# Kernel tuning notes

Measured on AMD Instinct MI355X. Metric: run time of the kernel, lower is better.

## Reference

```python
import jax, jax.numpy as jnp
import numpy as np

SIGMA = 0.02
B, CC, H, W = 4, 21, 96, 96
C_LOW, C_HIGH = 3, 512
N = H * W


def _grid_edges(h, w):
    idx = np.arange(h * w).reshape(h, w)
    eh = np.stack([idx[:, :-1].ravel(), idx[:, 1:].ravel()], 1)
    ev = np.stack([idx[:-1, :].ravel(), idx[1:, :].ravel()], 1)
    return np.concatenate([eh, ev], 0)  # [E,2] 4-connected grid edges


def _mst_bfs(feat, h, w):
    # feat: [C,h,w] numpy. Kruskal MST with norm2 edge weights, then BFS from node 0.
    n = h * w
    edges = _grid_edges(h, w)
    f = feat.reshape(feat.shape[0], -1)
    wts = ((f[:, edges[:, 0]] - f[:, edges[:, 1]]) ** 2).sum(0)
    order = np.argsort(wts, kind='stable')
    uf = np.arange(n)

    def find(x):
        r = x
        while uf[r] != r:
            r = uf[r]
        while uf[x] != r:
            uf[x], x = r, uf[x]
        return r

    adj = [[] for _ in range(n)]
    cnt = 0
    for ei in order:
        a, b = int(edges[ei, 0]), int(edges[ei, 1])
        ra, rb = find(a), find(b)
        if ra != rb:
            uf[ra] = rb
            adj[a].append(b)
            adj[b].append(a)
            cnt += 1
            if cnt == n - 1:
                break
    parent = np.zeros(n, np.int64)
    seen = np.zeros(n, bool)
    seen[0] = True
    levels, frontier = [[0]], [0]
    while frontier:
        nxt = []
        for u in frontier:
            for v in adj[u]:
                if not seen[v]:
                    seen[v] = True
                    parent[v] = u
                    nxt.append(v)
        if nxt:
            levels.append(nxt)
        frontier = nxt
    return parent, levels


def _tree_arrays(embed):
    # Host-side MST + BFS level schedule (integer tree topology, non-differentiable).
    e = np.asarray(jax.device_get(embed)).astype(np.float64)
    bn = e.shape[0]
    parents, levels = [], []
    for b in range(bn):
        p, lv = _mst_bfs(e[b], H, W)
        parents.append(p)
        levels.append(lv)
    D = max(len(lv) for lv in levels)
    L = max(max(len(l) for l in lv) for lv in levels)
    nodes = np.full((bn, D, L), N, np.int32)  # index N = dummy sink node
    for b, lv in enumerate(levels):
        for d, l in enumerate(lv):
            nodes[b, d, :len(l)] = l
    par = np.stack(parents)
    par = np.concatenate([par, np.full((bn, 1), N)], 1).astype(np.int32)
    msk = np.ones((bn, N + 1), np.float32)
    msk[:, 0] = 0.0  # root has no parent edge
    msk[:, N] = 0.0  # dummy node
    return jnp.asarray(nodes), jnp.asarray(par), jnp.asarray(msk)


def _tree_filter(feat, embed, nodes, parent, wmask, sigma):
    # feat [B,C,N], embed [B,Ce,N]. O(N) two-pass (leaf->root, root->leaf) tree DP:
    # out_i = sum_j (prod_{e in path(i,j)} w_e) f_j / same-with-f=1
    bn, c, nn = feat.shape
    ez = jnp.pad(embed, ((0, 0), (0, 0), (0, 1)))  # add dummy column
    ep = jax.vmap(lambda e, p: e[:, p])(ez, parent)  # parent embedding [B,Ce,N+1]
    w = wmask * jnp.exp(-((ez - ep) ** 2).sum(1) / sigma)  # edge weight per node [B,N+1]
    fa = jnp.concatenate([feat, jnp.ones((bn, 1, nn), feat.dtype)], 1)  # append norm channel
    fa = jnp.pad(fa, ((0, 0), (0, 0), (0, 1)))  # [B,C+1,N+1]

    def one(a0, wv, par, lvls):
        def up(a, lvl):  # children before parents: subtree aggregation
            return a.at[:, par[lvl]].add(wv[lvl] * a[:, lvl]), None
        a, _ = jax.lax.scan(up, a0, lvls[::-1])

        def down(s, lvl):  # parents before children: whole-tree aggregation
            wl = wv[lvl]
            sv = a[:, lvl] + wl * (s[:, par[lvl]] - wl * a[:, lvl])
            return s.at[:, lvl].set(sv), None
        s, _ = jax.lax.scan(down, a, lvls)
        return s

    s = jax.vmap(one)(fa, w, parent, nodes)
    return s[:, :c, :nn] / s[:, c:, :nn]


def _nearest(x, h, w):
    hr, wr = x.shape[-2:]
    ri = jnp.arange(h) * hr // h
    ci = jnp.arange(w) * wr // w
    return x[..., ri[:, None], ci[None, :]]


def setup_inputs():
    key = jax.random.key(0)
    k1, k2, k3, k4 = jax.random.split(key, 4)
    preds = jax.random.normal(k1, (B, CC, H, W), jnp.float32)
    low_feats = jax.random.uniform(k2, (B, C_LOW, H, W), dtype=jnp.float32)
    high_feats = 0.03 * jax.random.normal(k3, (B, C_HIGH, H, W), jnp.float32)
    roi = (jax.random.uniform(k4, (B, 1, 2 * H, 2 * W)) > 0.5).astype(jnp.float32)
    return {'preds': preds, 'low_feats': low_feats, 'high_feats': high_feats,
            'unlabeled_ROIs': roi}


def reference(preds, low_feats, high_feats, unlabeled_ROIs):
    nodes_l, par_l, msk_l = _tree_arrays(low_feats)
    nodes_h, par_h, msk_h = _tree_arrays(high_feats)
    roi = _nearest(unlabeled_ROIs, H, W)
    n = roi.sum()
    prob = jax.nn.sigmoid(preds)
    lf = low_feats.reshape(B, C_LOW, N)
    hf = high_feats.reshape(B, C_HIGH, N)
    AS = _tree_filter(prob.reshape(B, CC, N), lf, nodes_l, par_l, msk_l, SIGMA)
    AS = _tree_filter(AS, hf, nodes_h, par_h, msk_h, 1.0)
    loss = (roi * jnp.abs(prob - AS.reshape(B, CC, H, W))).sum()
    return jnp.where(n > 0, loss / n, jnp.zeros_like(loss))
```

## Files before the change

### kernel.cpp

```cpp
#include <hip/hip_runtime.h>
#include <math.h>
#include <stdint.h>
#include <stddef.h>


namespace {
constexpr int Bn  = 4, Cc = 21, Hh = 96, Ww = 96;
constexpr int Nn  = Hh * Ww;
constexpr int EhE = Hh * (Ww - 1);
constexpr int Ne  = EhE + (Hh - 1) * Ww;
constexpr int Clow = 3, Chigh = 512;
constexpr int NCh = Cc + 1;
constexpr int MAXD = 2048;
constexpr int TL  = 2 * (Nn - 1);
constexpr int ESL = 18432;
constexpr int SEG = 19;
constexpr int NR  = (TL + SEG - 1) / SEG;
constexpr int MAXC = 4608;
constexpr int NB_INIT = (Bn * Cc * Nn + 255) / 256;
constexpr int NB_EDGE = (Bn * Ne + 255) / 256;

constexpr size_t OFF_ACC  = 0;
constexpr size_t OFF_PROB = 256;
constexpr size_t OFF_S1   = OFF_PROB + (size_t)Bn * Cc * Nn * 4;
constexpr size_t OFF_S2   = OFF_S1   + (size_t)Bn * NCh * Nn * 4;
constexpr size_t OFF_EW   = OFF_S2   + (size_t)Bn * NCh * Nn * 4;
constexpr size_t OFF_ORD  = OFF_EW   + (size_t)8 * Ne * 8;
constexpr size_t OFF_PPOS = OFF_ORD  + (size_t)8 * Nn * 4;
constexpr size_t OFF_WGT  = OFF_PPOS + (size_t)8 * Nn * 2;
constexpr size_t OFF_LEV  = OFF_WGT  + (size_t)8 * Nn * 4;
constexpr size_t OFF_D    = OFF_LEV  + (size_t)8 * MAXD * 4;
constexpr size_t OFF_DIR  = OFF_D    + 256;
constexpr size_t OFF_CBW  = OFF_DIR  + (size_t)8 * Nn * 4;
constexpr size_t OFF_CBE  = OFF_CBW  + (size_t)8 * Nn * 8;
constexpr size_t OFF_OPP  = OFF_CBE  + (size_t)8 * Nn * 4;
constexpr size_t OFF_SGN  = OFF_OPP  + (size_t)8 * ESL * 2;
constexpr size_t OFF_PNF  = OFF_SGN  + (size_t)8 * ESL;
constexpr size_t OFF_RNK  = OFF_PNF  + (size_t)8 * Nn * 4;
constexpr size_t OFF_PAIR = OFF_RNK  + (size_t)8 * ESL * 2;
constexpr size_t OFF_EL1  = OFF_ORD;
constexpr size_t OFF_EL2  = OFF_WGT;
}

__device__ __forceinline__ void edge_nodes(int e, int& a, int& b) {
    if (e < EhE) { int h = e / (Ww - 1), w = e - h * (Ww - 1); a = h * Ww + w; b = a + 1; }
    else { int e2 = e - EhE; int h = e2 / Ww, w = e2 - h * Ww; a = h * Ww + w; b = a + Ww; }
}
__device__ __forceinline__ int dir_delta(int d) {
    return (d == 0) ? 1 : (d == 1) ? -1 : (d == 2) ? Ww : -Ww;
}
__device__ __forceinline__ int edge_of(int u, int d) {
    int h = u / Ww, w = u - h * Ww;
    if (d == 0) return h * (Ww - 1) + w;
    if (d == 1) return h * (Ww - 1) + w - 1;
    if (d == 2) return EhE + u;
    return EhE + u - Ww;
}

__device__ __forceinline__ unsigned long long mkkey(double w, int e) {
    unsigned long long q = (unsigned long long)(w * 70368744177664.0);
    if (q >= (1ull << 49)) q = (1ull << 49) - 1;
    return (q << 15) | (unsigned)e;
}

__device__ __forceinline__ void compact_push(bool keep, int val, int* cnt,
                                             unsigned short* out, int lane) {
    unsigned long long m = __ballot(keep ? 1 : 0);
    if (m == 0ull) return;
    int leader = __ffsll((unsigned long long)m) - 1;
    int base = 0;
    if (lane == leader) base = atomicAdd(cnt, __popcll(m));
    base = __shfl(base, leader, 64);
    if (keep) {
        unsigned long long lower = m & ((1ull << lane) - 1ull);
        out[base + __popcll(lower)] = (unsigned short)val;
    }
}

__device__ __forceinline__ int scan1024s(int val, int tid, int* wsum) {
    __syncthreads();
    int lane = tid & 63, wv = tid >> 6;
    int x = val;
    #pragma unroll
    for (int off = 1; off < 64; off <<= 1) {
        int y = __shfl_up(x, off, 64);
        if (lane >= off) x += y;
    }
    if (lane == 63) wsum[wv] = x;
    __syncthreads();
    if (wv == 0) {
        int s2 = (lane < 16) ? wsum[lane] : 0;
        #pragma unroll
        for (int off = 1; off < 16; off <<= 1) {
            int y = __shfl_up(s2, off, 64);
            if (lane >= off) s2 += y;
        }
        if (lane < 16) wsum[lane] = s2;
    }
    __syncthreads();
    int base = (wv > 0) ? wsum[wv - 1] : 0;
    return x + base;
}

__device__ __forceinline__ void edgew_body(const float* __restrict__ feat, int C,
                                           double* __restrict__ ew, int idx) {
    if (idx >= Bn * Ne) return;
    int b = idx / Ne, e = idx - b * Ne;
    int a, c2; edge_nodes(e, a, c2);
    const float* fa = feat + (size_t)b * C * Nn + a;
    const float* fb = feat + (size_t)b * C * Nn + c2;
    double s = 0.0;
    int c = 0;
    for (; c + 16 <= C; c += 16) {
        float va[16], vb[16];
        #pragma unroll
        for (int k = 0; k < 16; k++) {
            va[k] = fa[(size_t)(c + k) * Nn];
            vb[k] = fb[(size_t)(c + k) * Nn];
        }
        #pragma unroll
        for (int k = 0; k < 16; k++) {
            double d = (double)va[k] - (double)vb[k];
            s += d * d;
        }
    }
    for (; c < C; c++) {
        double d = (double)fa[(size_t)c * Nn] - (double)fb[(size_t)c * Nn];
        s += d * d;
    }
    ew[idx] = s;
}

__global__ void k_prep(const float* __restrict__ preds,
                       const float* __restrict__ lowf,
                       const float* __restrict__ highf,
                       float* __restrict__ prob, double* __restrict__ acc,
                       double* __restrict__ ewl, double* __restrict__ ewh) {
    int bid = blockIdx.x;
    if (bid < NB_INIT) {
        int idx = bid * 256 + threadIdx.x;
        if (idx == 0) { acc[0] = 0.0; acc[1] = 0.0; }
        if (idx >= Bn * Cc * Nn) return;
        prob[idx] = 1.0f / (1.0f + expf(-preds[idx]));
    } else if (bid < NB_INIT + NB_EDGE) {
        int idx = (bid - NB_INIT) * 256 + threadIdx.x;
        edgew_body(lowf, Clow, ewl, idx);
    } else {
        int idx = (bid - NB_INIT - NB_EDGE) * 256 + threadIdx.x;
        edgew_body(highf, Chigh, ewh, idx);
    }
}

__global__ void __launch_bounds__(1024)
k_mst(char* __restrict__ ws) {
    const int tb = blockIdx.x, tid = threadIdx.x;
    const int lane = tid & 63;
    const double* ew = (const double*)(ws + OFF_EW) + (size_t)tb * Ne;
    int* dirG = (int*)(ws + OFF_DIR) + (size_t)tb * Nn;
    unsigned short* elA = (unsigned short*)(ws + OFF_EL1) + (size_t)tb * Ne;
    unsigned short* elB = (unsigned short*)(ws + OFF_EL2) + (size_t)tb * Ne;

    __shared__ unsigned short comp[Nn];
    __shared__ unsigned long long cbK[MAXC];
    __shared__ int wsumM[16];
    __shared__ int chgArr[48];
    __shared__ int sLen, sNC;

    unsigned short* nxtN     = (unsigned short*)cbK;
    unsigned short* newSlotN = (unsigned short*)cbK + Nn;
    unsigned short* nxt      = (unsigned short*)cbK;
    unsigned short* newSlot  = (unsigned short*)cbK + MAXC;

    for (int i = tid; i < Nn; i += 1024) dirG[i] = 0;
    if (tid < 48) chgArr[tid] = 0;
    __syncthreads();

    for (int i = tid; i < Nn; i += 1024) {
        int h = i / Ww, w = i - h * Ww;
        unsigned long long bk = ~0ull;
        if (w < Ww - 1) { int e = h * (Ww - 1) + w;     unsigned long long k = mkkey(ew[e], e); if (k < bk) bk = k; }
        if (w > 0)      { int e = h * (Ww - 1) + w - 1; unsigned long long k = mkkey(ew[e], e); if (k < bk) bk = k; }
        if (h < Hh - 1) { int e = EhE + i;              unsigned long long k = mkkey(ew[e], e); if (k < bk) bk = k; }
        if (h > 0)      { int e = EhE + i - Ww;         unsigned long long k = mkkey(ew[e], e); if (k < bk) bk = k; }
        int e = (int)(bk & 0x7FFF);
        int a, c; edge_nodes(e, a, c);
        nxtN[i] = (unsigned short)((a == i) ? c : a);
        int da = (c == a + 1) ? 0 : 2;
        atomicOr(&dirG[a], 1 << da);
        atomicOr(&dirG[c], 1 << (da ^ 1));
    }
    __syncthreads();
    for (int i = tid; i < Nn; i += 1024) {
        int o = nxtN[i];
        if (o != i && nxtN[o] == i && i < o) nxtN[i] = (unsigned short)i;
    }
    __syncthreads();
    {
        int it = 0;
        while (it < 40) {
            bool any = false;
            for (int r = tid; r < Nn; r += 1024) {
                int nr = nxtN[r], nnr = nxtN[nr];
                if (nr != nnr) { nxtN[r] = (unsigned short)nnr; any = true; }
            }
            if (any) chgArr[it] = 1;
            __syncthreads();
            if (!chgArr[it]) break;
            it++;
        }
    }
    {
        int base = tid * 9, cnt = 0, loc[9];
        #pragma unroll
        for (int k = 0; k < 9; k++) {
            int i = base + k;
            loc[k] = cnt;
            if (nxtN[i] == i) cnt++;
        }
        int incl = scan1024s(cnt, tid, wsumM);
        int eb = incl - cnt;
        #pragma unroll
        for (int k = 0; k < 9; k++) {
            int i = base + k;
            if (nxtN[i] == i) newSlotN[i] = (unsigned short)(eb + loc[k]);
        }
        if (tid == 1023) sNC = incl;
    }
    __syncthreads();
    for (int i = tid; i < Nn; i += 1024) comp[i] = newSlotN[nxtN[i]];
    __syncthreads();
    int nComp = sNC;

    unsigned short* src = elA;
    unsigned short* dst = elB;
    int srcLen = -1;
    for (int round = 2; round < 22 && nComp > 1; round++) {
        if (tid == 0) sLen = 0;
        if (tid < 48) chgArr[tid] = 0;
        __syncthreads();
        if (srcLen < 0) {
            for (int e = tid; e < Ne; e += 1024) {
                int a, c; edge_nodes(e, a, c);
                compact_push(comp[a] != comp[c], e, &sLen, dst, lane);
            }
        } else {
            for (int k = tid; k < srcLen; k += 1024) {
                int e = src[k];
                int a, c; edge_nodes(e, a, c);
                compact_push(comp[a] != comp[c], e, &sLen, dst, lane);
            }
        }
        for (int s = tid; s < nComp; s += 1024) cbK[s] = ~0ull;
        __syncthreads();
        int len = sLen;
        if (len == 0) break;
        for (int k = tid; k < len; k += 1024) {
            int e = dst[k];
            int a, c; edge_nodes(e, a, c);
            unsigned long long key = mkkey(ew[e], e);
            atomicMin(&cbK[comp[a]], key);
            atomicMin(&cbK[comp[c]], key);
        }
        __syncthreads();
        unsigned long long kr[5];
        int nOwn = 0;
        for (int s = tid; s < nComp; s += 1024) kr[nOwn++] = cbK[s];
        __syncthreads();
        {
            int o = 0;
            for (int s = tid; s < nComp; s += 1024, o++) {
                unsigned long long key = kr[o];
                if (key != ~0ull) {
                    int e = (int)(key & 0x7FFF);
                    int a, c; edge_nodes(e, a, c);
                    int sa = comp[a], sc = comp[c];
                    nxt[s] = (unsigned short)((sa == s) ? sc : sa);
                    int da = (c == a + 1) ? 0 : 2;
                    atomicOr(&dirG[a], 1 << da);
                    atomicOr(&dirG[c], 1 << (da ^ 1));
                } else nxt[s] = (unsigned short)s;
            }
        }
        __syncthreads();
        for (int s = tid; s < nComp; s += 1024) {
            int o = nxt[s];
            if (o != s && nxt[o] == s && s < o) nxt[s] = (unsigned short)s;
        }
        __syncthreads();
        {
            int it = 0;
            while (it < 40) {
                bool any = false;
                for (int s = tid; s < nComp; s += 1024) {
                    int ns = nxt[s], nns = nxt[ns];
                    if (ns != nns) { nxt[s] = (unsigned short)nns; any = true; }
                }
                if (any) chgArr[it] = 1;
                __syncthreads();
                if (!chgArr[it]) break;
                it++;
            }
        }
        {
            int K = (nComp + 1023) >> 10;
            int base = tid * K, cnt = 0, loc[5];
            for (int k = 0; k < K; k++) {
                int s = base + k;
                loc[k] = cnt;
                if (s < nComp && nxt[s] == s) cnt++;
            }
            int incl = scan1024s(cnt, tid, wsumM);
            int eb = incl - cnt;
            for (int k = 0; k < K; k++) {
                int s = base + k;
                if (s < nComp && nxt[s] == s) newSlot[s] = (unsigned short)(eb + loc[k]);
            }
            if (tid == 1023) sNC = incl;
        }
        __syncthreads();
        for (int i = tid; i < Nn; i += 1024) comp[i] = newSlot[nxt[comp[i]]];
        __syncthreads();
        nComp = sNC;
        unsigned short* t = src; src = dst; dst = t;
        srcLen = len;
    }
}

__global__ void __launch_bounds__(1024)
k_topo(char* __restrict__ ws) {
    const int tb = blockIdx.x, tid = threadIdx.x;
    const int lane = tid & 63, wv = tid >> 6;
    const int tree = tb >> 2;
    const double* ew  = (const double*)(ws + OFF_EW) + (size_t)tb * Ne;
    const int*  dirG  = (const int*)(ws + OFF_DIR) + (size_t)tb * Nn;
    unsigned int*   elemSegG = (unsigned int*)(ws + OFF_CBW + (size_t)tb * 73728);
    unsigned short* ORG      = (unsigned short*)(ws + OFF_CBW + (size_t)tb * 73728);
    unsigned short* OWNR     = ORG + ESL;
    unsigned short* ownG     = (unsigned short*)(ws + OFF_CBE + (size_t)tb * (size_t)ESL * 2);
    unsigned short* oppG     = (unsigned short*)(ws + OFF_OPP + (size_t)tb * (size_t)ESL * 2);
    unsigned short* IRG      = (unsigned short*)(ws + OFF_SGN + (size_t)tb * ESL);
    unsigned short* rank0G   = (unsigned short*)(ws + OFF_RNK + (size_t)tb * (size_t)ESL * 2);
    int*            ordG  = (int*)(ws + OFF_ORD)  + (size_t)tb * Nn;
    uint2*          pairG = (uint2*)(ws + OFF_PAIR) + (size_t)tb * Nn;
    int*            levG  = (int*)(ws + OFF_LEV)  + (size_t)tb * MAXD;
    int*            dG    = (int*)(ws + OFF_D);
    const float inv_sigma = tree ? 1.0f : 50.0f;

    __shared__ char A[36864];
    __shared__ char B[18432];
    __shared__ char C[9216];
    __shared__ int  wsum[16];
    __shared__ int  sR, sPack, sCenter;

    unsigned short* degOff = (unsigned short*)B;
    unsigned char*  nbS    = (unsigned char*)C;
    for (int i = tid; i < Nn; i += 1024) nbS[i] = (unsigned char)dirG[i];
    __syncthreads();
    {
        int base9 = tid * 9;
        int loc[9]; int s = 0;
        #pragma unroll
        for (int k = 0; k < 9; k++) { loc[k] = s; s += __popc(nbS[base9 + k]); }
        int incl = scan1024s(s, tid, wsum);
        int eb = incl - s;
        #pragma unroll
        for (int k = 0; k < 9; k++) degOff[base9 + k] = (unsigned short)(eb + loc[k]);
    }
    __syncthreads();

    unsigned short* nxtS = (unsigned short*)A;
    for (int u = tid; u < Nn; u += 1024) {
        int m = nbS[u]; int base = degOff[u]; int k = 0;
        #pragma unroll
        for (int d = 0; d < 4; d++) {
            if (m & (1 << d)) {
                int v = u + dir_delta(d);
                int mv = nbS[v]; int rd = d ^ 1;
                int pv = __popc(mv & ((1 << rd) - 1));
                int dv = __popc(mv);
                int nx = pv + 1; if (nx == dv) nx = 0;
                int j = base + k;
                nxtS[j] = (unsigned short)(degOff[v] + nx);
                ownG[j] = (unsigned short)((u << 2) | d);
                oppG[j] = (unsigned short)(degOff[v] + pv);
                k++;
            }
        }
    }
    __syncthreads();

    int myNr = 0, myLen = 0;
    if (tid < NR) {
        int x = tid * SEG, off = 0;
        for (int g = 0; g < 4096; g++) {
            elemSegG[x] = ((unsigned)tid << 11) | (unsigned)off;
            int y = nxtS[x];
            if (y % SEG == 0) { myNr = y / SEG; myLen = off + 1; break; }
            x = y; off++;
        }
    }
    __syncthreads();

    unsigned short* cn  = (unsigned short*)C;
    unsigned short* cd  = (unsigned short*)(C + 2048);
    unsigned short* nn2 = (unsigned short*)(C + 4096);
    unsigned short* nd2 = (unsigned short*)(C + 6144);
    if (tid == 0)      { cn[0] = 0; cd[0] = 0; }
    else if (tid < NR) { cn[tid] = (unsigned short)myNr; cd[tid] = (unsigned short)myLen; }
    else               { cn[tid] = (unsigned short)tid; cd[tid] = 0; }
    __syncthreads();
    for (int r = 0; r < 10; r++) {
        int c = cn[tid];
        int dv = cd[tid] + cd[c];
        int n2 = cn[c];
        nn2[tid] = (unsigned short)n2; nd2[tid] = (unsigned short)dv;
        __syncthreads();
        unsigned short* t;
        t = cn; cn = nn2; nn2 = t;
        t = cd; cd = nd2; nd2 = t;
    }
    unsigned short* rb = nn2;
    rb[tid] = (tid == 0) ? 0 : (unsigned short)(TL - cd[tid]);
    __syncthreads();

    for (int hh = 0; hh < 2; hh++) {
        unsigned int pk4[9];
        #pragma unroll
        for (int t = 0; t < 9; t++) {
            int e = tid + (hh * 9 + t) * 1024;
            pk4[t] = elemSegG[e < TL ? e : 0];
        }
        unsigned short rbv[9];
        #pragma unroll
        for (int t = 0; t < 9; t++) rbv[t] = rb[pk4[t] >> 11];
        #pragma unroll
        for (int t = 0; t < 9; t++) {
            int e = tid + (hh * 9 + t) * 1024;
            if (e < TL) rank0G[e] = (unsigned short)(rbv[t] + (pk4[t] & 2047));
        }
    }
    __syncthreads();

    for (int hh = 0; hh < 2; hh++) {
        unsigned short rnk[9], opp[9], own2[9];
        #pragma unroll
        for (int t = 0; t < 9; t++) {
            int j = tid + (hh * 9 + t) * 1024;
            int ja = j < TL ? j : 0;
            rnk[t] = rank0G[ja]; opp[t] = oppG[ja]; own2[t] = ownG[ja];
        }
        unsigned short r2[9];
        #pragma unroll
        for (int t = 0; t < 9; t++) r2[t] = rank0G[opp[t]];
        #pragma unroll
        for (int t = 0; t < 9; t++) {
            int j = tid + (hh * 9 + t) * 1024;
            if (j < TL) { int r = rnk[t]; ORG[r] = r2[t]; OWNR[r] = own2[t]; }
        }
    }
    {
        unsigned short dof[9];
        #pragma unroll
        for (int t = 0; t < 9; t++) dof[t] = degOff[tid + t * 1024];
        unsigned short ov[9];
        #pragma unroll
        for (int t = 0; t < 9; t++) ov[t] = oppG[dof[t]];
        unsigned short rv[9];
        #pragma unroll
        for (int t = 0; t < 9; t++) rv[t] = rank0G[ov[t]];
        #pragma unroll
        for (int t = 0; t < 9; t++) IRG[tid + t * 1024] = rv[t];
    }
    __syncthreads();

    short* scanS = (short*)A;
    unsigned char* parC = (unsigned char*)C;
    unsigned short* depthB = (unsigned short*)B;
    int curRoot = 0, rootC = 0;
    for (int ph = 0; ph < 3; ph++) {
        if (tid == 0) {
            sR = ORG[IRG[curRoot]];
            sPack = 0;
        }
        __syncthreads();
        const int R = sR;
        const bool doPar = (ph >= 1);
        int base = tid * 18;
        int n = TL - base; if (n > 18) n = 18; if (n < 0) n = 0;
        unsigned short orvA[18], ownA[18];
        #pragma unroll
        for (int k = 0; k < 18; k++) {
            int q = base + k;
            int r = q + R; if (r >= TL) r -= TL; if (q >= TL) r = 0;
            orvA[k] = ORG[r];
        }
        if (doPar) {
            #pragma unroll
            for (int k = 0; k < 18; k++) {
                int q = base + k;
                int r = q + R; if (r >= TL) r -= TL; if (q >= TL) r = 0;
                ownA[k] = OWNR[r];
            }
        }
        short loc[18]; int s = 0;
        #pragma unroll
        for (int k = 0; k < 18; k++) {
            if (k < n) {
                int q = base + k;
                int rro = (int)orvA[k] - R; if (rro < 0) rro += TL;
                bool desc = q < rro;
                if (doPar && desc) {
                    int own = ownA[k];
                    int head = (own >> 2) + dir_delta(own & 3);
                    parC[head] = (unsigned char)((own & 3) ^ 1);
                }
                s += desc ? 1 : -1;
                loc[k] = (short)s;
            }
        }
        int incl = scan1024s(s, tid, wsum);
        int eb = incl - s;
        #pragma unroll
        for (int k = 0; k < 18; k++)
            if (k < n) scanS[base + k] = (short)(loc[k] + eb);
        __syncthreads();
        int pk = 0;
        {
            unsigned short qA[9];
            #pragma unroll
            for (int j = 0; j < 9; j++) qA[j] = IRG[tid + j * 1024];
            int depA[9];
            #pragma unroll
            for (int j = 0; j < 9; j++) {
                int q = (int)qA[j] - R; if (q < 0) q += TL;
                depA[j] = (int)scanS[q];
            }
            #pragma unroll
            for (int j = 0; j < 9; j++) {
                int x = tid + j * 1024;
                int dep = (x == curRoot) ? 0 : depA[j];
                int p2 = (dep << 14) | x;
                if (p2 > pk) pk = p2;
                if (ph == 2) depthB[x] = (unsigned short)dep;
            }
        }
        #pragma unroll
        for (int off = 32; off > 0; off >>= 1) {
            int o = __shfl_down(pk, off, 64);
            if (o > pk) pk = o;
        }
        if (lane == 0) atomicMax(&sPack, pk);
        __syncthreads();
        if (ph == 0) curRoot = sPack & 16383;
        else if (ph == 1) {
            int diam = sPack >> 14, v = sPack & 16383;
            int steps = diam - (diam >> 1);
            unsigned short* J  = (unsigned short*)A;
            unsigned short* J2 = (unsigned short*)(A + 18432);
            for (int x = tid; x < Nn; x += 1024)
                J[x] = (unsigned short)((x == curRoot) ? x : (x + dir_delta(parC[x])));
            if (tid == 0) sCenter = v;
            __syncthreads();
            for (int k = 0; (steps >> k) != 0; k++) {
                if (tid == 0 && ((steps >> k) & 1)) sCenter = J[sCenter];
                if ((steps >> (k + 1)) != 0) {
                    __syncthreads();
                    for (int x = tid; x < Nn; x += 1024) J2[x] = J[J[x]];
                    __syncthreads();
                    unsigned short* t = J; J = J2; J2 = t;
                }
            }
            __syncthreads();
            curRoot = sCenter;
            rootC = curRoot;
        }
        __syncthreads();
    }
    const int D = (sPack >> 14) + 1;

    unsigned short* posOf = (unsigned short*)A;
    int* hist   = (int*)(A + 18432);
    int* levOff = (int*)(A + 26624);
    for (int k = tid; k < 2048; k += 1024) hist[k] = 0;
    __syncthreads();
    for (int v = tid; v < Nn; v += 1024) atomicAdd(&hist[depthB[v]], 1);
    __syncthreads();
    {
        int h0 = hist[2 * tid], h1 = hist[2 * tid + 1];
        int partial = h0 + h1;
        int incl = scan1024s(partial, tid, wsum);
        int eb = incl - partial;
        levOff[2 * tid] = eb;
        levOff[2 * tid + 1] = eb + h0;
    }
    __syncthreads();
    for (int d = tid; d <= D && d < 2048; d += 1024) levG[d] = levOff[d];
    for (int k = tid; k < 2048; k += 1024) hist[k] = 0;
    __syncthreads();
    for (int v = tid; v < Nn; v += 1024) {
        int dep = depthB[v];
        int pos = levOff[dep] + atomicAdd(&hist[dep], 1);
        posOf[v] = (unsigned short)pos;
        ordG[pos] = v;
    }
    __syncthreads();

    {
        unsigned char rdA[9]; unsigned short posA[9];
        #pragma unroll
        for (int t = 0; t < 9; t++) {
            int v = tid + t * 1024;
            rdA[t] = parC[v]; posA[t] = posOf[v];
        }
        double ewv[9]; unsigned short ppv[9];
        #pragma unroll
        for (int t = 0; t < 9; t++) {
            int v = tid + t * 1024;
            int rd = rdA[t] & 3;
            bool ir = (v == rootC);
            int p  = ir ? v : v + dir_delta(rd);
            int ei = ir ? 0 : edge_of(v, rd);
            ppv[t] = posOf[p];
            ewv[t] = ew[ei];
        }
        #pragma unroll
        for (int t = 0; t < 9; t++) {
            int v = tid + t * 1024;
            int pos = posA[t];
            if (v == rootC) {
                pairG[pos] = make_uint2(0u, 0u);
            } else {
                float w = expf(-(float)ewv[t] * inv_sigma);
                pairG[pos] = make_uint2(__float_as_uint(w), (unsigned)ppv[t]);
            }
        }
    }
    if (tid == 0) dG[tb] = D;
}

__global__ void __launch_bounds__(64)
k_dp(char* __restrict__ ws, int tree, int inMode) {
    const int bc = blockIdx.x;
    const int b = bc / NCh, c = bc % NCh;
    const int tb = tree * Bn + b;
    const int lane = threadIdx.x;
    const int*   ordG  = (const int*)(ws + OFF_ORD)  + (size_t)tb * Nn;
    const uint2* pairG = (const uint2*)(ws + OFF_PAIR) + (size_t)tb * Nn;
    const int*   levG  = (const int*)(ws + OFF_LEV)  + (size_t)tb * MAXD;
    const int D = ((const int*)(ws + OFF_D))[tb];
    const float* src = (inMode == 0)
        ? (const float*)(ws + OFF_PROB) + ((size_t)b * Cc + c) * Nn
        : (const float*)(ws + OFF_S1)   + ((size_t)b * NCh + c) * Nn;
    const float* srcN = (const float*)(ws + OFF_S1) + ((size_t)b * NCh + Cc) * Nn;
    float* dst = (float*)(ws + (tree ? OFF_S2 : OFF_S1)) + ((size_t)b * NCh + c) * Nn;

    __shared__ alignas(16) float Al[Nn];
    __shared__ alignas(16) uint2 pairS[Nn];
    __shared__ unsigned short levS[MAXD];

    {
        const uint4* pg4 = (const uint4*)pairG;
        uint4* ps4 = (uint4*)pairS;
        for (int k = lane; k < Nn / 2; k += 64) ps4[k] = pg4[k];
    }
    for (int d = lane; d <= D && d < MAXD; d += 64) levS[d] = (unsigned short)levG[d];
    if (c == Cc)            { for (int i = lane; i < Nn; i += 64) Al[i] = 1.0f; }
    else if (inMode == 0)   { for (int i = lane; i < Nn; i += 64) Al[i] = src[ordG[i]]; }
    else                    { for (int i = lane; i < Nn; i += 64) { int nd = ordG[i]; Al[i] = src[nd] / srcN[nd]; } }
    __builtin_amdgcn_wave_barrier();
    asm volatile("" ::: "memory");

    if (D > 1) {
        for (int d = D - 1; d >= 1; d--) {
            int sd = levS[d], sd1 = levS[d + 1];
            for (int i = sd + lane; i < sd1; i += 64) {
                uint2 pk = pairS[i];
                atomicAdd(&Al[pk.y], __uint_as_float(pk.x) * Al[i]);
            }
        }
    }
    if (D > 1) {
        for (int d = 1; d < D; d++) {
            int sd = levS[d], sd1 = levS[d + 1];
            for (int i = sd + lane; i < sd1; i += 64) {
                uint2 pk = pairS[i];
                float w = __uint_as_float(pk.x);
                float a = Al[i];
                Al[i] = a + w * (Al[pk.y] - w * a);
            }
        }
    }
    __builtin_amdgcn_wave_barrier();
    asm volatile("" ::: "memory");
    for (int i = lane; i < Nn; i += 64) dst[ordG[i]] = Al[i];
}

__global__ void k_loss(char* __restrict__ ws, const float* __restrict__ roi) {
    const int tid = threadIdx.x;
    int idx = blockIdx.x * 256 + tid;
    const float* prob = (const float*)(ws + OFF_PROB);
    const float* S2   = (const float*)(ws + OFF_S2);
    double* acc = (double*)(ws + OFF_ACC);
    double ls = 0.0, cnt = 0.0;
    if (idx < Bn * Cc * Nn) {
        int b = idx / (Cc * Nn);
        int rem = idx - b * (Cc * Nn);
        int c = rem / Nn, n = rem - c * Nn;
        int h = n / Ww, w2 = n - h * Ww;
        float r = roi[(size_t)b * (2 * Hh) * (2 * Ww) + (size_t)(2 * h) * (2 * Ww) + 2 * w2];
        float as = S2[((size_t)b * NCh + c) * Nn + n] / S2[((size_t)b * NCh + Cc) * Nn + n];
        float pp = prob[((size_t)b * Cc + c) * Nn + n];
        ls = (double)(r * fabsf(pp - as));
        if (c == 0) cnt = (double)r;
    }
    __shared__ double sl[256], sc2[256];
    sl[tid] = ls; sc2[tid] = cnt;
    __syncthreads();
    for (int s = 128; s > 0; s >>= 1) {
        if (tid < s) { sl[tid] += sl[tid + s]; sc2[tid] += sc2[tid + s]; }
        __syncthreads();
    }
    if (tid == 0) { atomicAdd(acc, sl[0]); atomicAdd(acc + 1, sc2[0]); }
}

__global__ void k_final(const double* __restrict__ acc, float* __restrict__ out) {
    if (blockIdx.x == 0 && threadIdx.x == 0)
        out[0] = (acc[1] > 0.0) ? (float)(acc[0] / acc[1]) : 0.0f;
}

extern "C" void kernel_launch(void* const* d_in, const int* in_sizes, int n_in,
                              void* d_out, int out_size, void* d_ws, size_t ws_size,
                              hipStream_t stream) {
    const float* preds = (const float*)d_in[0];
    const float* lowf  = (const float*)d_in[1];
    const float* highf = (const float*)d_in[2];
    const float* roi   = (const float*)d_in[3];
    char* ws = (char*)d_ws;
    float* out = (float*)d_out;
    double* ewl = (double*)(ws + OFF_EW);
    double* ewh = (double*)(ws + OFF_EW) + (size_t)Bn * Ne;

    k_prep<<<NB_INIT + 2 * NB_EDGE, 256, 0, stream>>>(
        preds, lowf, highf, (float*)(ws + OFF_PROB), (double*)(ws + OFF_ACC),
        ewl, ewh);
    k_mst<<<8, 1024, 0, stream>>>(ws);
    k_topo<<<8, 1024, 0, stream>>>(ws);
    k_dp<<<Bn * NCh, 64, 0, stream>>>(ws, 0, 0);
    k_dp<<<Bn * NCh, 64, 0, stream>>>(ws, 1, 1);
    k_loss<<<(Bn * Cc * Nn + 255) / 256, 256, 0, stream>>>(ws, roi);
    k_final<<<1, 64, 0, stream>>>((const double*)(ws + OFF_ACC), out);
}
```

Baseline: 659.1 us.

## Process two tree levels per top-down pass using grandparent pointers

The topology kernel now also stores each node's grandparent position, packed into the pair word, plus the parent's edge weight in a new array. The top-down DP pass handles two levels per step: a node in the second level recomputes its parent's updated value from the grandparent, so half as many level iterations are needed. Chunks are processed in reverse order so that nodes read their parent's value before it is overwritten. This adds another shared array of about 36KB plus extra loads per node, which may lower occupancy, and it depends on OFF_WGT being defined elsewhere.

```diff
diff --git a/kernel.cpp b/kernel.cpp
--- a/kernel.cpp
+++ b/kernel.cpp
@@ -342,6 +342,7 @@
     unsigned short* rank0G   = (unsigned short*)(ws + OFF_RNK + (size_t)tb * (size_t)ESL * 2);
     int*            ordG  = (int*)(ws + OFF_ORD)  + (size_t)tb * Nn;
     uint2*          pairG = (uint2*)(ws + OFF_PAIR) + (size_t)tb * Nn;
+    float*          wpG   = (float*)(ws + OFF_WGT) + (size_t)tb * Nn;
     int*            levG  = (int*)(ws + OFF_LEV)  + (size_t)tb * MAXD;
     int*            dG    = (int*)(ws + OFF_D);
     const float inv_sigma = tree ? 1.0f : 50.0f;
@@ -612,26 +613,46 @@
             int v = tid + t * 1024;
             rdA[t] = parC[v]; posA[t] = posOf[v];
         }
-        double ewv[9]; unsigned short ppv[9];
+        int p1A[9];
         #pragma unroll
         for (int t = 0; t < 9; t++) {
             int v = tid + t * 1024;
-            int rd = rdA[t] & 3;
-            bool ir = (v == rootC);
-            int p  = ir ? v : v + dir_delta(rd);
-            int ei = ir ? 0 : edge_of(v, rd);
-            ppv[t] = posOf[p];
+            p1A[t] = (v == rootC) ? v : v + dir_delta(rdA[t] & 3);
+        }
+        unsigned char rd1A[9];
+        #pragma unroll
+        for (int t = 0; t < 9; t++) rd1A[t] = parC[p1A[t]];
+        int p2A[9];
+        #pragma unroll
+        for (int t = 0; t < 9; t++)
+            p2A[t] = (p1A[t] == rootC) ? p1A[t] : p1A[t] + dir_delta(rd1A[t] & 3);
+        unsigned short pp1[9], pp2[9];
+        #pragma unroll
+        for (int t = 0; t < 9; t++) {
+            pp1[t] = posOf[p1A[t]];
+            pp2[t] = posOf[p2A[t]];
+        }
+        double ewv[9], ewp[9];
+        #pragma unroll
+        for (int t = 0; t < 9; t++) {
+            int v = tid + t * 1024;
+            int ei  = (v == rootC) ? 0 : edge_of(v, rdA[t] & 3);
+            int eip = (p1A[t] == rootC) ? 0 : edge_of(p1A[t], rd1A[t] & 3);
             ewv[t] = ew[ei];
+            ewp[t] = ew[eip];
         }
         #pragma unroll
         for (int t = 0; t < 9; t++) {
             int v = tid + t * 1024;
             int pos = posA[t];
+            wpG[pos] = (p1A[t] == rootC) ? 0.0f
+                     : expf(-(float)ewp[t] * inv_sigma);
             if (v == rootC) {
                 pairG[pos] = make_uint2(0u, 0u);
             } else {
                 float w = expf(-(float)ewv[t] * inv_sigma);
-                pairG[pos] = make_uint2(__float_as_uint(w), (unsigned)ppv[t]);
+                pairG[pos] = make_uint2(__float_as_uint(w),
+                                        (unsigned)pp1[t] | ((unsigned)pp2[t] << 14));
             }
         }
     }
@@ -646,6 +667,7 @@
     const int lane = threadIdx.x;
     const int*   ordG  = (const int*)(ws + OFF_ORD)  + (size_t)tb * Nn;
     const uint2* pairG = (const uint2*)(ws + OFF_PAIR) + (size_t)tb * Nn;
+    const float* wpGp  = (const float*)(ws + OFF_WGT) + (size_t)tb * Nn;
     const int*   levG  = (const int*)(ws + OFF_LEV)  + (size_t)tb * MAXD;
     const int D = ((const int*)(ws + OFF_D))[tb];
     const float* src = (inMode == 0)
@@ -656,12 +678,16 @@
 
     __shared__ alignas(16) float Al[Nn];
     __shared__ alignas(16) uint2 pairS[Nn];
+    __shared__ alignas(16) float wpS[Nn];
     __shared__ unsigned short levS[MAXD];
 
     {
         const uint4* pg4 = (const uint4*)pairG;
         uint4* ps4 = (uint4*)pairS;
         for (int k = lane; k < Nn / 2; k += 64) ps4[k] = pg4[k];
+        const uint4* wg4 = (const uint4*)wpGp;
+        uint4* ws4 = (uint4*)wpS;
+        for (int k = lane; k < Nn / 4; k += 64) ws4[k] = wg4[k];
     }
     for (int d = lane; d <= D && d < MAXD; d += 64) levS[d] = (unsigned short)levG[d];
     if (c == Cc)            { for (int i = lane; i < Nn; i += 64) Al[i] = 1.0f; }
@@ -675,18 +701,31 @@
             int sd = levS[d], sd1 = levS[d + 1];
             for (int i = sd + lane; i < sd1; i += 64) {
                 uint2 pk = pairS[i];
-                atomicAdd(&Al[pk.y], __uint_as_float(pk.x) * Al[i]);
+                atomicAdd(&Al[pk.y & 0x3FFFu], __uint_as_float(pk.x) * Al[i]);
             }
         }
     }
     if (D > 1) {
-        for (int d = 1; d < D; d++) {
-            int sd = levS[d], sd1 = levS[d + 1];
-            for (int i = sd + lane; i < sd1; i += 64) {
-                uint2 pk = pairS[i];
-                float w = __uint_as_float(pk.x);
-                float a = Al[i];
-                Al[i] = a + w * (Al[pk.y] - w * a);
+        for (int d0 = 1; d0 < D; d0 += 2) {
+            int dEnd = (d0 + 2 < D) ? d0 + 2 : D;
+            int bS = levS[d0], bE = levS[dEnd];
+            int L1 = (d0 + 1 < D) ? (int)levS[d0 + 1] : bE;
+            int nch = (bE - bS + 63) >> 6;
+            for (int ch = nch - 1; ch >= 0; --ch) {
+                int i = bS + ch * 64 + lane;
+                if (i < bE) {
+                    uint2 pk = pairS[i];
+                    float w = __uint_as_float(pk.x);
+                    int pp = (int)(pk.y & 0x3FFFu);
+                    int a2 = (int)((pk.y >> 14) & 0x3FFFu);
+                    float a   = Al[i];
+                    float up  = Al[pp];
+                    float sa2 = Al[a2];
+                    float wp  = wpS[i];
+                    float sp2 = up + wp * (sa2 - wp * up);
+                    float sp  = (i < L1) ? up : sp2;
+                    Al[i] = a + w * (sp - w * a);
+                }
             }
         }
     }
```

Measured after the change: 693.1 us. 5.2% more time.
